# Kernel tuning notes

Hardware: AMD Instinct MI355X
Metric: run time of the kernel (lower is better)

## Reference

```python
import jax, jax.numpy as jnp
import numpy as np

B, CQ, CKV, H, W = 8, 256, 512, 64, 64
HKV, WKV = 32, 32
DQK = CQ // 8  # 32


def setup_inputs() -> dict:
    key = jax.random.key(0)
    ks = jax.random.split(key, 9)
    s = 0.05
    return {
        "query": jax.random.normal(ks[0], (B, CQ, H, W), jnp.float32),
        "key_value": jax.random.normal(ks[1], (B, CKV, HKV, WKV), jnp.float32),
        "Wq": jax.random.normal(ks[2], (DQK, CQ), jnp.float32) * s,
        "bq": jax.random.normal(ks[3], (DQK,), jnp.float32) * s,
        "Wk": jax.random.normal(ks[4], (DQK, CKV), jnp.float32) * s,
        "bk": jax.random.normal(ks[5], (DQK,), jnp.float32) * s,
        "Wv": jax.random.normal(ks[6], (CQ, CKV), jnp.float32) * s,
        "bv": jax.random.normal(ks[7], (CQ,), jnp.float32) * s,
        "gamma": jax.random.normal(ks[8], (1,), jnp.float32) * 0.5,
    }


def reference(query, key_value, Wq, bq, Wk, bk, Wv, bv, gamma):
    b, cq, h, w = query.shape
    n = h * w
    # bilinear resize of key_value to query's spatial size (align_corners=False
    # half-pixel convention, matching torch F.interpolate and jax.image.resize)
    kv = jax.image.resize(key_value, (b, key_value.shape[1], h, w), method="bilinear")
    # 1x1 convs are channel contractions
    q = jnp.einsum("bchw,dc->bdhw", query, Wq) + bq[None, :, None, None]   # [B,DQK,H,W]
    k = jnp.einsum("bchw,dc->bdhw", kv, Wk) + bk[None, :, None, None]      # [B,DQK,H,W]
    v = jnp.einsum("bchw,dc->bdhw", kv, Wv) + bv[None, :, None, None]      # [B,CQ,H,W]
    qf = q.reshape(b, -1, n)   # [B,DQK,N]
    kf = k.reshape(b, -1, n)   # [B,DQK,N]
    vf = v.reshape(b, -1, n)   # [B,CQ,N]
    energy = jnp.einsum("bdn,bdm->bnm", qf, kf)        # [B,N,N]
    attention = jax.nn.softmax(energy, axis=-1)
    out = jnp.einsum("bnm,bcm->bcn", attention, vf)     # [B,CQ,N]
    out = out.reshape(b, cq, h, w)
    return gamma[0] * out + query
```

## Files before the change

### kernel.cpp

```cpp
#include <hip/hip_runtime.h>

#define B_ 8
#define CQ_ 256
#define CKV_ 512
#define N_ 4096
#define DQK_ 32

typedef __bf16 bf16;
typedef __bf16 bf16x4 __attribute__((ext_vector_type(4)));
typedef __bf16 bf16x8 __attribute__((ext_vector_type(8)));
typedef float f32x4 __attribute__((ext_vector_type(4)));

__global__ void k_convert_w(const float* __restrict__ Wq, const float* __restrict__ Wk,
                            const float* __restrict__ Wv,
                            bf16* __restrict__ wq, bf16* __restrict__ wk, bf16* __restrict__ wv) {
    int i = blockIdx.x * 256 + threadIdx.x;
    if (i < 8192) wq[i] = (bf16)Wq[i];
    else if (i < 24576) wk[i - 8192] = (bf16)Wk[i - 8192];
    else if (i < 155648) wv[i - 24576] = (bf16)Wv[i - 24576];
}

__global__ __launch_bounds__(256) void k_resize(const float* __restrict__ kv, bf16* __restrict__ kvr) {
    const int yo = blockIdx.x;
    const int b  = blockIdx.y;
    const int tid = threadIdx.x;
    __shared__ float r0[64][33];
    __shared__ float r1[64][33];
    int ty = yo >> 1;
    int y0, y1; float wy0, wy1;
    if ((yo & 1) == 0) { y0 = ty > 0 ? ty - 1 : 0; y1 = ty; wy0 = 0.25f; wy1 = 0.75f; }
    else               { y0 = ty; y1 = ty < 31 ? ty + 1 : 31; wy0 = 0.75f; wy1 = 0.25f; }
    const int u_loc = tid & 63;
    const int xo_base = tid >> 6;
    for (int uc = 0; uc < CKV_; uc += 64) {
        __syncthreads();
        for (int i = 0; i < 8; ++i) {
            int idx = tid + i * 256;
            int u = idx >> 5, x = idx & 31;
            const float* src = kv + ((size_t)b * CKV_ + uc + u) * 1024 + x;
            r0[u][x] = src[y0 * 32];
            r1[u][x] = src[y1 * 32];
        }
        __syncthreads();
        for (int i = 0; i < 16; ++i) {
            int xo = xo_base + i * 4;
            int tx = xo >> 1;
            int xa, xb; float wxa, wxb;
            if ((xo & 1) == 0) { xa = tx > 0 ? tx - 1 : 0; xb = tx; wxa = 0.25f; wxb = 0.75f; }
            else               { xa = tx; xb = tx < 31 ? tx + 1 : 31; wxa = 0.75f; wxb = 0.25f; }
            float v0 = wxa * r0[u_loc][xa] + wxb * r0[u_loc][xb];
            float v1 = wxa * r1[u_loc][xa] + wxb * r1[u_loc][xb];
            float val = wy0 * v0 + wy1 * v1;
            kvr[((size_t)b * N_ + yo * 64 + xo) * CKV_ + uc + u_loc] = (bf16)val;
        }
    }
}

__global__ __launch_bounds__(256) void k_proj_q_fused(const float* __restrict__ query,
                                                      const bf16* __restrict__ W,
                                                      const float* __restrict__ bias,
                                                      bf16* __restrict__ qTb) {
    __shared__ bf16 tile[64][264];
    const int n0 = blockIdx.x * 64;
    const int b  = blockIdx.y;
    const int tid = threadIdx.x;
    const int xi = tid & 15, c0 = tid >> 4;
    for (int pass = 0; pass < 16; ++pass) {
        int c = c0 + pass * 16;
        const float4 v = *(const float4*)(query + ((size_t)b * CQ_ + c) * N_ + n0 + xi * 4);
        tile[xi * 4 + 0][c] = (bf16)v.x;
        tile[xi * 4 + 1][c] = (bf16)v.y;
        tile[xi * 4 + 2][c] = (bf16)v.z;
        tile[xi * 4 + 3][c] = (bf16)v.w;
    }
    __syncthreads();
    const int w = tid >> 6, lane = tid & 63;
    const int l16 = lane & 15, quad = lane >> 4;
    const int ct = w & 1, nh = w >> 1;
    f32x4 acc[2];
    acc[0] = (f32x4){0.f, 0.f, 0.f, 0.f}; acc[1] = (f32x4){0.f, 0.f, 0.f, 0.f};
    const bf16* aptr = W + (ct * 16 + l16) * CQ_ + quad * 8;
#pragma unroll
    for (int ks = 0; ks < 8; ++ks) {
        bf16x8 af = *(const bf16x8*)(aptr + ks * 32);
        for (int j = 0; j < 2; ++j) {
            bf16x8 bfv = *(const bf16x8*)&tile[nh * 32 + j * 16 + l16][ks * 32 + quad * 8];
            acc[j] = __builtin_amdgcn_mfma_f32_16x16x32_bf16(af, bfv, acc[j], 0, 0, 0);
        }
    }
    for (int j = 0; j < 2; ++j)
        for (int r = 0; r < 4; ++r) {
            int d = ct * 16 + quad * 4 + r;
            int n = n0 + nh * 32 + j * 16 + l16;
            qTb[((size_t)b * N_ + n) * DQK_ + d] = (bf16)(acc[j][r] + bias[d]);
        }
}

__global__ __launch_bounds__(256) void k_proj_k(const bf16* __restrict__ W,
                                                const float* __restrict__ bias,
                                                const bf16* __restrict__ Bm,
                                                bf16* __restrict__ outT) {
    const int mb = blockIdx.x * 128;
    const int b  = blockIdx.y;
    const int tid = threadIdx.x;
    const int w = tid >> 6, lane = tid & 63;
    const int l16 = lane & 15, quad = lane >> 4;
    const int ct = w & 1;
    const int mhalf = (w >> 1) * 64;
    f32x4 acc[4];
    for (int j = 0; j < 4; ++j) acc[j] = (f32x4){0.f, 0.f, 0.f, 0.f};
    const bf16* aptr  = W + (ct * 16 + l16) * CKV_ + quad * 8;
    const bf16* bbase = Bm + ((size_t)b * N_ + mb + mhalf) * CKV_ + quad * 8;
#pragma unroll
    for (int ks = 0; ks < 16; ++ks) {
        bf16x8 af = *(const bf16x8*)(aptr + ks * 32);
        for (int j = 0; j < 4; ++j) {
            bf16x8 bfv = *(const bf16x8*)(bbase + (size_t)(j * 16 + l16) * CKV_ + ks * 32);
            acc[j] = __builtin_amdgcn_mfma_f32_16x16x32_bf16(af, bfv, acc[j], 0, 0, 0);
        }
    }
    for (int j = 0; j < 4; ++j)
        for (int r = 0; r < 4; ++r) {
            int d = ct * 16 + quad * 4 + r;
            int m = mb + mhalf + j * 16 + l16;
            outT[((size_t)b * N_ + m) * DQK_ + d] = (bf16)(acc[j][r] + bias[d]);
        }
}

__global__ __launch_bounds__(256) void k_proj_v(const bf16* __restrict__ W,
                                                const float* __restrict__ bias,
                                                const bf16* __restrict__ Bm,
                                                bf16* __restrict__ vout) {
    const int mb = blockIdx.x * 64;
    const int b  = blockIdx.y;
    const int tid = threadIdx.x;
    const int w = tid >> 6, lane = tid & 63;
    const int l16 = lane & 15, quad = lane >> 4;
    f32x4 acc[4][4];
    for (int i = 0; i < 4; ++i) for (int j = 0; j < 4; ++j) acc[i][j] = (f32x4){0.f, 0.f, 0.f, 0.f};
    const bf16* bbase = Bm + ((size_t)b * N_ + mb) * CKV_ + quad * 8;
#pragma unroll 4
    for (int ks = 0; ks < 16; ++ks) {
        bf16x8 bfv[4];
        for (int j = 0; j < 4; ++j)
            bfv[j] = *(const bf16x8*)(bbase + (size_t)(j * 16 + l16) * CKV_ + ks * 32);
        for (int i = 0; i < 4; ++i) {
            bf16x8 af = *(const bf16x8*)(W + (size_t)((w * 4 + i) * 16 + l16) * CKV_ + ks * 32 + quad * 8);
            for (int j = 0; j < 4; ++j)
                acc[i][j] = __builtin_amdgcn_mfma_f32_16x16x32_bf16(af, bfv[j], acc[i][j], 0, 0, 0);
        }
    }
    for (int i = 0; i < 4; ++i)
        for (int r = 0; r < 4; ++r) {
            int c = (w * 4 + i) * 16 + quad * 4 + r;
            float bvs = bias[c];
            for (int j = 0; j < 4; ++j) {
                int m = mb + j * 16 + l16;
                vout[((size_t)b * CQ_ + c) * N_ + m] = (bf16)(acc[i][j][r] + bvs);
            }
        }
}

__global__ __launch_bounds__(256) void k_flash(const bf16* __restrict__ qT,
                                               const bf16* __restrict__ kT,
                                               const bf16* __restrict__ vv,
                                               const float* __restrict__ query,
                                               const float* __restrict__ gamma,
                                               float* __restrict__ out) {
    __shared__ bf16 P[2][64][72];
    __shared__ float linvs[64];
    const int b  = blockIdx.y;
    const int n0 = blockIdx.x * 64;
    const int tid = threadIdx.x;
    const int w = tid >> 6, lane = tid & 63;
    const int l16 = lane & 15, quad = lane >> 4;
    const int swz = l16 & 3;

    const bf16x8 qfrag = *(const bf16x8*)(qT + ((size_t)b * N_ + n0 + w * 16 + l16) * DQK_ + quad * 8);

    f32x4 acc[4][4];
    for (int i = 0; i < 4; ++i) for (int j = 0; j < 4; ++j) acc[i][j] = (f32x4){0.f, 0.f, 0.f, 0.f};
    f32x4 lsum = (f32x4){0.f, 0.f, 0.f, 0.f};

    const bf16* kbase = kT + (size_t)b * N_ * DQK_;
    const bf16* vbase = vv + ((size_t)b * CQ_ + w * 64) * N_;

    bf16x8 kf[4];
    for (int im = 0; im < 4; ++im)
        kf[im] = *(const bf16x8*)(kbase + (size_t)(im * 16 + l16) * DQK_ + quad * 8);

    for (int mt = 0; mt < 64; ++mt) {
        const int m0 = mt * 64;
        bf16 (* __restrict__ Pb)[72] = P[mt & 1];
        for (int im = 0; im < 4; ++im) {
            f32x4 s = __builtin_amdgcn_mfma_f32_16x16x32_bf16(kf[im], qfrag,
                                                              (f32x4){0.f, 0.f, 0.f, 0.f}, 0, 0, 0);
            bf16x4 pk;
            for (int r = 0; r < 4; ++r) {
                float p = __expf(s[r]);
                lsum[r] += p;
                pk[r] = (bf16)p;
            }
            *(bf16x4*)&Pb[w * 16 + l16][((im ^ swz) << 4) + quad * 4] = pk;
        }
        bf16x8 vf[2][4];
        for (int ks = 0; ks < 2; ++ks)
            for (int i = 0; i < 4; ++i)
                vf[ks][i] = *(const bf16x8*)(vbase + (size_t)(i * 16 + l16) * N_ + m0 + ks * 32 + quad * 8);
        const int m1 = (mt + 1 < 64 ? mt + 1 : 0) * 64;
        bf16x8 kn[4];
        for (int im = 0; im < 4; ++im)
            kn[im] = *(const bf16x8*)(kbase + (size_t)(m1 + im * 16 + l16) * DQK_ + quad * 8);
        __syncthreads();
        for (int ks = 0; ks < 2; ++ks) {
            bf16x8 pf[4];
            for (int j = 0; j < 4; ++j)
                pf[j] = *(const bf16x8*)&Pb[j * 16 + l16]
                            [((((ks << 1) | (quad >> 1)) ^ swz) << 4) + ((quad & 1) << 3)];
            for (int i = 0; i < 4; ++i)
                for (int j = 0; j < 4; ++j)
                    acc[i][j] = __builtin_amdgcn_mfma_f32_16x16x32_bf16(vf[ks][i], pf[j], acc[i][j], 0, 0, 0);
        }
        for (int im = 0; im < 4; ++im) kf[im] = kn[im];
    }
    float s = (lsum[0] + lsum[1]) + (lsum[2] + lsum[3]);
    s += __shfl_xor(s, 16);
    s += __shfl_xor(s, 32);
    if (quad == 0) linvs[w * 16 + l16] = 1.f / s;
    __syncthreads();
    float linv[4];
    for (int j = 0; j < 4; ++j) linv[j] = linvs[j * 16 + l16];
    const float g = gamma[0];
    for (int i = 0; i < 4; ++i)
        for (int r = 0; r < 4; ++r) {
            int c = w * 64 + i * 16 + quad * 4 + r;
            for (int j = 0; j < 4; ++j) {
                int n = n0 + j * 16 + l16;
                size_t idx = ((size_t)b * CQ_ + c) * N_ + n;
                out[idx] = g * acc[i][j][r] * linv[j] + query[idx];
            }
        }
}

extern "C" void kernel_launch(void* const* d_in, const int* in_sizes, int n_in,
                              void* d_out, int out_size, void* d_ws, size_t ws_size,
                              hipStream_t stream) {
    const float* query     = (const float*)d_in[0];
    const float* key_value = (const float*)d_in[1];
    const float* Wq = (const float*)d_in[2];
    const float* bq = (const float*)d_in[3];
    const float* Wk = (const float*)d_in[4];
    const float* bk = (const float*)d_in[5];
    const float* Wv = (const float*)d_in[6];
    const float* bv = (const float*)d_in[7];
    const float* gamma = (const float*)d_in[8];
    float* out = (float*)d_out;

    char* ws = (char*)d_ws;
    bf16* kvr  = (bf16*)(ws);
    bf16* vbuf = (bf16*)(ws + 33554432);
    bf16* qTb  = (bf16*)(ws + 50331648);
    bf16* kTb  = (bf16*)(ws + 52428800);
    bf16* wqb  = (bf16*)(ws + 54525952);
    bf16* wkb  = (bf16*)(ws + 54542336);
    bf16* wvb  = (bf16*)(ws + 54575104);

    k_convert_w<<<608, 256, 0, stream>>>(Wq, Wk, Wv, wqb, wkb, wvb);
    k_resize<<<dim3(64, 8), 256, 0, stream>>>(key_value, kvr);
    k_proj_q_fused<<<dim3(64, 8), 256, 0, stream>>>(query, wqb, bq, qTb);
    k_proj_k<<<dim3(32, 8), 256, 0, stream>>>(wkb, bk, kvr, kTb);
    k_proj_v<<<dim3(64, 8), 256, 0, stream>>>(wvb, bv, kvr, vbuf);
    k_flash<<<dim3(64, 8), 256, 0, stream>>>(qTb, kTb, vbuf, query, gamma, out);
}
```

Before: 341.8 us.

## Split flash KV loop across two wave groups, widen grids, use exp2 softmax

The flash kernel now runs 512 threads per block: two groups of four waves each take alternating KV tiles, and their partial accumulators and row sums are combined through shared memory at the end. It also raises MFMA wave priority and remaps the block order so batches interleave. Softmax uses exp2 with log2(e) folded into Wq and bq. Resize, K-projection and V-projection grids are made finer for more parallelism. The cost is extra reduction traffic, barriers and register pressure in the flash kernel.

```diff
diff --git a/kernel.cpp b/kernel.cpp
--- a/kernel.cpp
+++ b/kernel.cpp
@@ -5,6 +5,7 @@
 #define CKV_ 512
 #define N_ 4096
 #define DQK_ 32
+#define LOG2E 1.44269504f
 
 typedef __bf16 bf16;
 typedef __bf16 bf16x4 __attribute__((ext_vector_type(4)));
@@ -15,7 +16,7 @@
                             const float* __restrict__ Wv,
                             bf16* __restrict__ wq, bf16* __restrict__ wk, bf16* __restrict__ wv) {
     int i = blockIdx.x * 256 + threadIdx.x;
-    if (i < 8192) wq[i] = (bf16)Wq[i];
+    if (i < 8192) wq[i] = (bf16)(Wq[i] * LOG2E);
     else if (i < 24576) wk[i - 8192] = (bf16)Wk[i - 8192];
     else if (i < 155648) wv[i - 24576] = (bf16)Wv[i - 24576];
 }
@@ -23,6 +24,7 @@
 __global__ __launch_bounds__(256) void k_resize(const float* __restrict__ kv, bf16* __restrict__ kvr) {
     const int yo = blockIdx.x;
     const int b  = blockIdx.y;
+    const int uc = blockIdx.z * 64;
     const int tid = threadIdx.x;
     __shared__ float r0[64][33];
     __shared__ float r1[64][33];
@@ -32,27 +34,24 @@
     else               { y0 = ty; y1 = ty < 31 ? ty + 1 : 31; wy0 = 0.75f; wy1 = 0.25f; }
     const int u_loc = tid & 63;
     const int xo_base = tid >> 6;
-    for (int uc = 0; uc < CKV_; uc += 64) {
-        __syncthreads();
-        for (int i = 0; i < 8; ++i) {
-            int idx = tid + i * 256;
-            int u = idx >> 5, x = idx & 31;
-            const float* src = kv + ((size_t)b * CKV_ + uc + u) * 1024 + x;
-            r0[u][x] = src[y0 * 32];
-            r1[u][x] = src[y1 * 32];
-        }
-        __syncthreads();
-        for (int i = 0; i < 16; ++i) {
-            int xo = xo_base + i * 4;
-            int tx = xo >> 1;
-            int xa, xb; float wxa, wxb;
-            if ((xo & 1) == 0) { xa = tx > 0 ? tx - 1 : 0; xb = tx; wxa = 0.25f; wxb = 0.75f; }
-            else               { xa = tx; xb = tx < 31 ? tx + 1 : 31; wxa = 0.75f; wxb = 0.25f; }
-            float v0 = wxa * r0[u_loc][xa] + wxb * r0[u_loc][xb];
-            float v1 = wxa * r1[u_loc][xa] + wxb * r1[u_loc][xb];
-            float val = wy0 * v0 + wy1 * v1;
-            kvr[((size_t)b * N_ + yo * 64 + xo) * CKV_ + uc + u_loc] = (bf16)val;
-        }
+    for (int i = 0; i < 8; ++i) {
+        int idx = tid + i * 256;
+        int u = idx >> 5, x = idx & 31;
+        const float* src = kv + ((size_t)b * CKV_ + uc + u) * 1024 + x;
+        r0[u][x] = src[y0 * 32];
+        r1[u][x] = src[y1 * 32];
+    }
+    __syncthreads();
+    for (int i = 0; i < 16; ++i) {
+        int xo = xo_base + i * 4;
+        int tx = xo >> 1;
+        int xa, xb; float wxa, wxb;
+        if ((xo & 1) == 0) { xa = tx > 0 ? tx - 1 : 0; xb = tx; wxa = 0.25f; wxb = 0.75f; }
+        else               { xa = tx; xb = tx < 31 ? tx + 1 : 31; wxa = 0.75f; wxb = 0.25f; }
+        float v0 = wxa * r0[u_loc][xa] + wxb * r0[u_loc][xb];
+        float v1 = wxa * r1[u_loc][xa] + wxb * r1[u_loc][xb];
+        float val = wy0 * v0 + wy1 * v1;
+        kvr[((size_t)b * N_ + yo * 64 + xo) * CKV_ + uc + u_loc] = (bf16)val;
     }
 }
 
@@ -92,7 +91,7 @@
         for (int r = 0; r < 4; ++r) {
             int d = ct * 16 + quad * 4 + r;
             int n = n0 + nh * 32 + j * 16 + l16;
-            qTb[((size_t)b * N_ + n) * DQK_ + d] = (bf16)(acc[j][r] + bias[d]);
+            qTb[((size_t)b * N_ + n) * DQK_ + d] = (bf16)(acc[j][r] + bias[d] * LOG2E);
         }
 }
 
@@ -100,53 +99,51 @@
                                                 const float* __restrict__ bias,
                                                 const bf16* __restrict__ Bm,
                                                 bf16* __restrict__ outT) {
-    const int mb = blockIdx.x * 128;
-    const int b  = blockIdx.y;
+    const int flat = blockIdx.x + 128 * blockIdx.y;
+    const int b  = flat & 7;
+    const int mb = (flat >> 3) * 32;
     const int tid = threadIdx.x;
     const int w = tid >> 6, lane = tid & 63;
     const int l16 = lane & 15, quad = lane >> 4;
     const int ct = w & 1;
-    const int mhalf = (w >> 1) * 64;
-    f32x4 acc[4];
-    for (int j = 0; j < 4; ++j) acc[j] = (f32x4){0.f, 0.f, 0.f, 0.f};
-    const bf16* aptr  = W + (ct * 16 + l16) * CKV_ + quad * 8;
-    const bf16* bbase = Bm + ((size_t)b * N_ + mb + mhalf) * CKV_ + quad * 8;
+    const int mh = (w >> 1) * 16;
+    f32x4 acc = (f32x4){0.f, 0.f, 0.f, 0.f};
+    const bf16* aptr = W + (ct * 16 + l16) * CKV_ + quad * 8;
+    const bf16* bptr = Bm + ((size_t)b * N_ + mb + mh + l16) * CKV_ + quad * 8;
 #pragma unroll
     for (int ks = 0; ks < 16; ++ks) {
-        bf16x8 af = *(const bf16x8*)(aptr + ks * 32);
-        for (int j = 0; j < 4; ++j) {
-            bf16x8 bfv = *(const bf16x8*)(bbase + (size_t)(j * 16 + l16) * CKV_ + ks * 32);
-            acc[j] = __builtin_amdgcn_mfma_f32_16x16x32_bf16(af, bfv, acc[j], 0, 0, 0);
-        }
-    }
-    for (int j = 0; j < 4; ++j)
-        for (int r = 0; r < 4; ++r) {
-            int d = ct * 16 + quad * 4 + r;
-            int m = mb + mhalf + j * 16 + l16;
-            outT[((size_t)b * N_ + m) * DQK_ + d] = (bf16)(acc[j][r] + bias[d]);
-        }
+        bf16x8 af  = *(const bf16x8*)(aptr + ks * 32);
+        bf16x8 bfv = *(const bf16x8*)(bptr + ks * 32);
+        acc = __builtin_amdgcn_mfma_f32_16x16x32_bf16(af, bfv, acc, 0, 0, 0);
+    }
+    const int m = mb + mh + l16;
+    for (int r = 0; r < 4; ++r) {
+        int d = ct * 16 + quad * 4 + r;
+        outT[((size_t)b * N_ + m) * DQK_ + d] = (bf16)(acc[r] + bias[d]);
+    }
 }
 
 __global__ __launch_bounds__(256) void k_proj_v(const bf16* __restrict__ W,
                                                 const float* __restrict__ bias,
                                                 const bf16* __restrict__ Bm,
                                                 bf16* __restrict__ vout) {
-    const int mb = blockIdx.x * 64;
-    const int b  = blockIdx.y;
+    const int flat = blockIdx.x + 128 * blockIdx.y;
+    const int b  = flat & 7;
+    const int mb = (flat >> 3) * 32;
     const int tid = threadIdx.x;
     const int w = tid >> 6, lane = tid & 63;
     const int l16 = lane & 15, quad = lane >> 4;
-    f32x4 acc[4][4];
-    for (int i = 0; i < 4; ++i) for (int j = 0; j < 4; ++j) acc[i][j] = (f32x4){0.f, 0.f, 0.f, 0.f};
+    f32x4 acc[4][2];
+    for (int i = 0; i < 4; ++i) for (int j = 0; j < 2; ++j) acc[i][j] = (f32x4){0.f, 0.f, 0.f, 0.f};
     const bf16* bbase = Bm + ((size_t)b * N_ + mb) * CKV_ + quad * 8;
 #pragma unroll 4
     for (int ks = 0; ks < 16; ++ks) {
-        bf16x8 bfv[4];
-        for (int j = 0; j < 4; ++j)
+        bf16x8 bfv[2];
+        for (int j = 0; j < 2; ++j)
             bfv[j] = *(const bf16x8*)(bbase + (size_t)(j * 16 + l16) * CKV_ + ks * 32);
         for (int i = 0; i < 4; ++i) {
             bf16x8 af = *(const bf16x8*)(W + (size_t)((w * 4 + i) * 16 + l16) * CKV_ + ks * 32 + quad * 8);
-            for (int j = 0; j < 4; ++j)
+            for (int j = 0; j < 2; ++j)
                 acc[i][j] = __builtin_amdgcn_mfma_f32_16x16x32_bf16(af, bfv[j], acc[i][j], 0, 0, 0);
         }
     }
@@ -154,64 +151,75 @@
         for (int r = 0; r < 4; ++r) {
             int c = (w * 4 + i) * 16 + quad * 4 + r;
             float bvs = bias[c];
-            for (int j = 0; j < 4; ++j) {
+            for (int j = 0; j < 2; ++j) {
                 int m = mb + j * 16 + l16;
                 vout[((size_t)b * CQ_ + c) * N_ + m] = (bf16)(acc[i][j][r] + bvs);
             }
         }
 }
 
-__global__ __launch_bounds__(256) void k_flash(const bf16* __restrict__ qT,
-                                               const bf16* __restrict__ kT,
-                                               const bf16* __restrict__ vv,
-                                               const float* __restrict__ query,
-                                               const float* __restrict__ gamma,
-                                               float* __restrict__ out) {
-    __shared__ bf16 P[2][64][72];
-    __shared__ float linvs[64];
-    const int b  = blockIdx.y;
-    const int n0 = blockIdx.x * 64;
-    const int tid = threadIdx.x;
-    const int w = tid >> 6, lane = tid & 63;
+__global__ __launch_bounds__(512, 4) void k_flash(const bf16* __restrict__ qT,
+                                                  const bf16* __restrict__ kT,
+                                                  const bf16* __restrict__ vv,
+                                                  const float* __restrict__ query,
+                                                  const float* __restrict__ gamma,
+                                                  float* __restrict__ out) {
+    __shared__ bf16 P[2][2][64][72];
+    __shared__ float lpart[2][64];
+    const int tid = threadIdx.x;
+    const int w8 = tid >> 6;
+    const int h  = w8 >> 2;
+    const int w  = w8 & 3;
+    const int lane = tid & 63;
     const int l16 = lane & 15, quad = lane >> 4;
     const int swz = l16 & 3;
+    const int flat = blockIdx.x + 64 * blockIdx.y;
+    const int b  = flat & 7;
+    const int n0 = (flat >> 3) * 64;
 
     const bf16x8 qfrag = *(const bf16x8*)(qT + ((size_t)b * N_ + n0 + w * 16 + l16) * DQK_ + quad * 8);
 
-    f32x4 acc[4][4];
-    for (int i = 0; i < 4; ++i) for (int j = 0; j < 4; ++j) acc[i][j] = (f32x4){0.f, 0.f, 0.f, 0.f};
+    f32x4 acc[16];
+#pragma unroll
+    for (int i = 0; i < 16; ++i) acc[i] = (f32x4){0.f, 0.f, 0.f, 0.f};
     f32x4 lsum = (f32x4){0.f, 0.f, 0.f, 0.f};
 
     const bf16* kbase = kT + (size_t)b * N_ * DQK_;
     const bf16* vbase = vv + ((size_t)b * CQ_ + w * 64) * N_;
 
+    auto loadK = [&](int mt, bf16x8* dst) {
+        for (int im = 0; im < 4; ++im)
+            dst[im] = *(const bf16x8*)(kbase + (size_t)(mt * 64 + im * 16 + l16) * DQK_ + quad * 8);
+    };
+
     bf16x8 kf[4];
-    for (int im = 0; im < 4; ++im)
-        kf[im] = *(const bf16x8*)(kbase + (size_t)(im * 16 + l16) * DQK_ + quad * 8);
-
-    for (int mt = 0; mt < 64; ++mt) {
+    loadK(h, kf);
+
+#pragma unroll 2
+    for (int t = 0; t < 32; ++t) {
+        const int mt = 2 * t + h;
         const int m0 = mt * 64;
-        bf16 (* __restrict__ Pb)[72] = P[mt & 1];
+        bf16x8 vf[2][4];
+        for (int ks = 0; ks < 2; ++ks)
+            for (int i = 0; i < 4; ++i)
+                vf[ks][i] = *(const bf16x8*)(vbase + (size_t)(i * 16 + l16) * N_ + m0 + ks * 32 + quad * 8);
+        bf16x8 kn[4];
+        loadK(mt + 2 < 64 ? mt + 2 : 0, kn);
+        bf16 (* __restrict__ Pb)[72] = P[h][t & 1];
         for (int im = 0; im < 4; ++im) {
             f32x4 s = __builtin_amdgcn_mfma_f32_16x16x32_bf16(kf[im], qfrag,
                                                               (f32x4){0.f, 0.f, 0.f, 0.f}, 0, 0, 0);
             bf16x4 pk;
             for (int r = 0; r < 4; ++r) {
-                float p = __expf(s[r]);
+                float p = exp2f(s[r]);
                 lsum[r] += p;
                 pk[r] = (bf16)p;
             }
             *(bf16x4*)&Pb[w * 16 + l16][((im ^ swz) << 4) + quad * 4] = pk;
         }
-        bf16x8 vf[2][4];
-        for (int ks = 0; ks < 2; ++ks)
-            for (int i = 0; i < 4; ++i)
-                vf[ks][i] = *(const bf16x8*)(vbase + (size_t)(i * 16 + l16) * N_ + m0 + ks * 32 + quad * 8);
-        const int m1 = (mt + 1 < 64 ? mt + 1 : 0) * 64;
-        bf16x8 kn[4];
-        for (int im = 0; im < 4; ++im)
-            kn[im] = *(const bf16x8*)(kbase + (size_t)(m1 + im * 16 + l16) * DQK_ + quad * 8);
+        for (int im = 0; im < 4; ++im) kf[im] = kn[im];
         __syncthreads();
+        __builtin_amdgcn_s_setprio(1);
         for (int ks = 0; ks < 2; ++ks) {
             bf16x8 pf[4];
             for (int j = 0; j < 4; ++j)
@@ -219,25 +227,50 @@
                             [((((ks << 1) | (quad >> 1)) ^ swz) << 4) + ((quad & 1) << 3)];
             for (int i = 0; i < 4; ++i)
                 for (int j = 0; j < 4; ++j)
-                    acc[i][j] = __builtin_amdgcn_mfma_f32_16x16x32_bf16(vf[ks][i], pf[j], acc[i][j], 0, 0, 0);
-        }
-        for (int im = 0; im < 4; ++im) kf[im] = kn[im];
-    }
-    float s = (lsum[0] + lsum[1]) + (lsum[2] + lsum[3]);
-    s += __shfl_xor(s, 16);
-    s += __shfl_xor(s, 32);
-    if (quad == 0) linvs[w * 16 + l16] = 1.f / s;
+                    acc[i * 4 + j] = __builtin_amdgcn_mfma_f32_16x16x32_bf16(vf[ks][i], pf[j], acc[i * 4 + j], 0, 0, 0);
+        }
+        __builtin_amdgcn_s_setprio(0);
+    }
+
+    float sden = (lsum[0] + lsum[1]) + (lsum[2] + lsum[3]);
+    sden += __shfl_xor(sden, 16);
+    sden += __shfl_xor(sden, 32);
+    if (lane < 16) lpart[h][w * 16 + l16] = sden;
     __syncthreads();
-    float linv[4];
-    for (int j = 0; j < 4; ++j) linv[j] = linvs[j * 16 + l16];
+
+    float* fb = (float*)&P[0][0][0][0];
+    for (int pass = 0; pass < 2; ++pass) {
+        const int ibase = pass * 2;
+        for (int i = 0; i < 2; ++i)
+            for (int jj = 0; jj < 2; ++jj) {
+                int jg = (h == 0) ? 2 + jj : jj;
+                int slot = ((i * 2 + jj) * 512 + w8 * 64 + lane) * 4;
+                *(f32x4*)&fb[slot] = acc[(ibase + i) * 4 + jg];
+            }
+        __syncthreads();
+        for (int i = 0; i < 2; ++i)
+            for (int jj = 0; jj < 2; ++jj) {
+                int jk = (h == 0) ? jj : 2 + jj;
+                int slot = ((i * 2 + jj) * 512 + (w8 ^ 4) * 64 + lane) * 4;
+                acc[(ibase + i) * 4 + jk] += *(const f32x4*)&fb[slot];
+            }
+        __syncthreads();
+    }
+
+    float linv[2];
+    for (int jj = 0; jj < 2; ++jj) {
+        int jk = (h == 0) ? jj : 2 + jj;
+        linv[jj] = 1.f / (lpart[0][jk * 16 + l16] + lpart[1][jk * 16 + l16]);
+    }
     const float g = gamma[0];
     for (int i = 0; i < 4; ++i)
         for (int r = 0; r < 4; ++r) {
             int c = w * 64 + i * 16 + quad * 4 + r;
-            for (int j = 0; j < 4; ++j) {
-                int n = n0 + j * 16 + l16;
+            for (int jj = 0; jj < 2; ++jj) {
+                int jk = (h == 0) ? jj : 2 + jj;
+                int n = n0 + jk * 16 + l16;
                 size_t idx = ((size_t)b * CQ_ + c) * N_ + n;
-                out[idx] = g * acc[i][j][r] * linv[j] + query[idx];
+                out[idx] = g * acc[i * 4 + jk][r] * linv[jj] + query[idx];
             }
         }
 }
@@ -266,9 +299,9 @@
     bf16* wvb  = (bf16*)(ws + 54575104);
 
     k_convert_w<<<608, 256, 0, stream>>>(Wq, Wk, Wv, wqb, wkb, wvb);
-    k_resize<<<dim3(64, 8), 256, 0, stream>>>(key_value, kvr);
+    k_resize<<<dim3(64, 8, 8), 256, 0, stream>>>(key_value, kvr);
     k_proj_q_fused<<<dim3(64, 8), 256, 0, stream>>>(query, wqb, bq, qTb);
-    k_proj_k<<<dim3(32, 8), 256, 0, stream>>>(wkb, bk, kvr, kTb);
-    k_proj_v<<<dim3(64, 8), 256, 0, stream>>>(wvb, bv, kvr, vbuf);
-    k_flash<<<dim3(64, 8), 256, 0, stream>>>(qTb, kTb, vbuf, query, gamma, out);
-}
+    k_proj_k<<<dim3(128, 8), 256, 0, stream>>>(wkb, bk, kvr, kTb);
+    k_proj_v<<<dim3(128, 8), 256, 0, stream>>>(wvb, bv, kvr, vbuf);
+    k_flash<<<dim3(64, 8), 512, 0, stream>>>(qTb, kTb, vbuf, query, gamma, out);
+}
```

After: 600.7 us. 75.7% more time.
